# Performance work log

Measured on AMD Instinct MI355X. Metric: run time of the kernel, lower is better.

The kernel has to match this reference:

```python
import jax, jax.numpy as jnp
import numpy as np

LAMBDA1 = 0.3366
LAMBDA2 = 0.2424
LAMBDA3 = 0.06
LR = 0.1
N_ITERS = 10          # fixed iteration count standing in for the eps-based while loop
BETA1, BETA2, ADAM_EPS = 0.9, 0.999, 1e-8


def setup_inputs() -> dict:
    key = jax.random.key(0)
    k1, k2, k3 = jax.random.split(key, 3)
    D, T, K = 512, 50000, 16
    return {
        "embedding": jax.random.normal(k1, (D, T), jnp.float32),
        "basis_init": jax.random.normal(k2, (D, K), jnp.float32),
        "activation_init": jax.random.normal(k3, (K, T), jnp.float32),
        "k": K,
    }


def _matrix_l1(X):
    # torch.linalg.norm(X, ord=1) on a 2D tensor = induced 1-norm = max column abs-sum
    return jnp.max(jnp.sum(jnp.abs(X), axis=0))


def _jitter(A):
    # temporal jitter penalty: sum of abs frame-to-frame differences
    return jnp.sum(jnp.abs(A[:, 1:] - A[:, :-1]))


def _shrink(X):
    # faithful to the (buggy) torch _shrink: sign(X) * max(0, |X - lr*l|)
    return jnp.sign(X) * jnp.maximum(0.0, jnp.abs(X - LR * LAMBDA1))


def _adam(p, g, m, v, t):
    m = BETA1 * m + (1.0 - BETA1) * g
    v = BETA2 * v + (1.0 - BETA2) * g * g
    mh = m / (1.0 - BETA1 ** t)
    vh = v / (1.0 - BETA2 ** t)
    p = p - LR * mh / (jnp.sqrt(vh) + ADAM_EPS)
    return p, m, v


def _run(embedding, basis_init, activation_init):
    A = activation_init  # optimizer_act.step() is never called in the source -> A is constant

    def loss_from_B(B):
        return (_matrix_l1(embedding - B @ A)
                + LAMBDA1 * _matrix_l1(B)
                + LAMBDA2 * _matrix_l1(A)
                + LAMBDA3 * _jitter(A))

    # iteration 1: loss is computed on the raw parameter (shrink applied after the step)
    P = basis_init
    m = jnp.zeros_like(P)
    v = jnp.zeros_like(P)
    g = jax.grad(loss_from_B)(P)
    P, m, v = _adam(P, g, m, v, jnp.float32(1.0))

    # iterations 2..N: loss sees shrink(P); gradient flows through the shrink into P
    def step(carry, t):
        P, m, v = carry
        g = jax.grad(lambda p: loss_from_B(_shrink(p)))(P)
        P, m, v = _adam(P, g, m, v, t)
        return (P, m, v), None

    ts = jnp.arange(2, N_ITERS + 1, dtype=jnp.float32)
    (P, m, v), _ = jax.lax.scan(step, (P, m, v), ts)
    return _shrink(P), A


def reference(embedding, basis_init, activation_init, k):
    # returns (embedding_basis_matrix, activation_matrix) as in OutputDiarization
    return _run(embedding, basis_init, activation_init)
```

## Files before the change

### kernel.cpp

```cpp
#include <hip/hip_runtime.h>
#include <hip/hip_cooperative_groups.h>

namespace cg = cooperative_groups;

#define D 512
#define T 50000
#define K 16
#define NIT 10

#define NBLK 256
#define BTH  512
#define COLS_PER_BLOCK 196
#define NGRP 49
#define PASSES 2

#define LAMBDA1 0.3366f
#define LR      0.1f
#define SHRINK_C (LR * LAMBDA1)
#define BETA1   0.9f
#define BETA2   0.999f
#define ADAM_EPS 1e-8f

__device__ __forceinline__ float sgn(float x) {
    return (x > 0.f) ? 1.f : ((x < 0.f) ? -1.f : 0.f);
}

__global__ __launch_bounds__(BTH, 2) void diar_all(
        const float* __restrict__ E, const float* __restrict__ Bin,
        const float* __restrict__ A, float* __restrict__ out,
        unsigned long long* __restrict__ slot) {
    __shared__ __align__(16) float Bl[D * K];
    __shared__ float4 psum[16][32];
    __shared__ float wsum[8][K];
    __shared__ float colA[K];
    __shared__ int js_s, ks_s;

    const int tid = threadIdx.x;
    const int bid = blockIdx.x;
    cg::grid_group grid = cg::this_grid();

    float pr[K], mr[K], vr[K];
    {
        const float4* src = reinterpret_cast<const float4*>(Bin + tid * K);
        float4* bl4 = reinterpret_cast<float4*>(&Bl[tid * K]);
#pragma unroll
        for (int q = 0; q < 4; ++q) {
            float4 x = src[q];
            bl4[q] = x;
            pr[4 * q + 0] = x.x; pr[4 * q + 1] = x.y;
            pr[4 * q + 2] = x.z; pr[4 * q + 3] = x.w;
        }
#pragma unroll
        for (int k = 0; k < K; ++k) { mr[k] = 0.f; vr[k] = 0.f; }
    }
    if (bid == 0 && tid < NIT) atomicExch(&slot[tid], 0ull);
    __syncthreads();
    grid.sync();

    const int c = tid & 31;
    const int s = tid >> 5;

    float b1p = 1.f, b2p = 1.f;

    for (int it = 1; it <= NIT; ++it) {
        b1p *= BETA1; b2p *= BETA2;

        unsigned long long key = 0ull;
#pragma unroll
        for (int p = 0; p < PASSES; ++p) {
            const int g = p * 32 + c;
            const int j0 = bid * COLS_PER_BLOCK + g * 4;
            const bool ok = (g < NGRP) && (j0 < T);
            float4 acc = {0.f, 0.f, 0.f, 0.f};
            if (ok) {
                float4 a4[K];
#pragma unroll
                for (int k = 0; k < K; ++k)
                    a4[k] = *reinterpret_cast<const float4*>(A + (size_t)k * T + j0);
                const int rbase = s * 32;
                const float* Ep = E + j0;
#pragma unroll 4
                for (int ii = 0; ii < 32; ++ii) {
                    const int i = rbase + ii;
                    const float4 e = *reinterpret_cast<const float4*>(Ep + (size_t)i * T);
                    const float4* br = reinterpret_cast<const float4*>(&Bl[i * K]);
                    float bb[K];
                    *reinterpret_cast<float4*>(&bb[0])  = br[0];
                    *reinterpret_cast<float4*>(&bb[4])  = br[1];
                    *reinterpret_cast<float4*>(&bb[8])  = br[2];
                    *reinterpret_cast<float4*>(&bb[12]) = br[3];
                    float4 r = e;
#pragma unroll
                    for (int k = 0; k < K; ++k) {
                        r.x = fmaf(-bb[k], a4[k].x, r.x);
                        r.y = fmaf(-bb[k], a4[k].y, r.y);
                        r.z = fmaf(-bb[k], a4[k].z, r.z);
                        r.w = fmaf(-bb[k], a4[k].w, r.w);
                    }
                    acc.x += fabsf(r.x); acc.y += fabsf(r.y);
                    acc.z += fabsf(r.z); acc.w += fabsf(r.w);
                }
            }
            psum[s][c] = acc;
            __syncthreads();
            if (tid < 32) {
                const int gg = p * 32 + tid;
                const int jb = bid * COLS_PER_BLOCK + gg * 4;
                if (gg < NGRP && jb < T) {
                    float4 cs = psum[0][tid];
#pragma unroll
                    for (int q = 1; q < 16; ++q) {
                        float4 pq = psum[q][tid];
                        cs.x += pq.x; cs.y += pq.y; cs.z += pq.z; cs.w += pq.w;
                    }
                    float v4[4] = {cs.x, cs.y, cs.z, cs.w};
#pragma unroll
                    for (int q = 0; q < 4; ++q) {
                        unsigned long long kq =
                            (((unsigned long long)__float_as_uint(v4[q])) << 32)
                            | (unsigned int)(jb + q);
                        if (kq > key) key = kq;
                    }
                }
            }
            __syncthreads();
        }
        if (tid < 64) {
#pragma unroll
            for (int off = 32; off > 0; off >>= 1) {
                unsigned long long o = __shfl_down(key, off, 64);
                if (o > key) key = o;
            }
            if (tid == 0) atomicMax(&slot[it - 1], key);
        }

        grid.sync();

        if (tid == 0) {
            unsigned long long kk = atomicMax(&slot[it - 1], 0ull);
            js_s = (int)(kk & 0xffffffffull);
        }
        __syncthreads();
        const int js = js_s;
        if (tid < K) colA[tid] = A[(size_t)tid * T + js];

        float cb[K];
        {
            const float* brow = &Bl[tid * K];
#pragma unroll
            for (int k = 0; k < K; ++k) cb[k] = fabsf(brow[k]);
#pragma unroll
            for (int off = 32; off > 0; off >>= 1) {
#pragma unroll
                for (int k = 0; k < K; ++k) cb[k] += __shfl_down(cb[k], off, 64);
            }
            if ((tid & 63) == 0) {
                const int w = tid >> 6;
#pragma unroll
                for (int k = 0; k < K; ++k) wsum[w][k] = cb[k];
            }
        }
        __syncthreads();
        if (tid == 0) {
            float best = -1.f; int kb = 0;
#pragma unroll
            for (int k = 0; k < K; ++k) {
                float t = 0.f;
                for (int w = 0; w < 8; ++w) t += wsum[w][k];
                if (t > best) { best = t; kb = k; }
            }
            ks_s = kb;
        }
        __syncthreads();
        const int ks = ks_s;
        const float biasm = 1.f - b1p;
        const float biasv = 1.f - b2p;

        float r = E[(size_t)tid * T + js];
        const float* brow = &Bl[tid * K];
#pragma unroll
        for (int k = 0; k < K; ++k) r = fmaf(-brow[k], colA[k], r);
        const float sg = sgn(r);

#pragma unroll
        for (int k = 0; k < K; ++k) {
            float g = -sg * colA[k];
            if (k == ks) g += LAMBDA1 * sgn(brow[k]);
            float p = pr[k];
            if (it >= 2) g *= sgn(p) * sgn(p - SHRINK_C);
            float mm = BETA1 * mr[k] + (1.f - BETA1) * g;
            float vv = BETA2 * vr[k] + (1.f - BETA2) * g * g;
            mr[k] = mm; vr[k] = vv;
            p -= LR * (mm / biasm) / (sqrtf(vv / biasv) + ADAM_EPS);
            pr[k] = p;
        }
        {
            float4* bl4 = reinterpret_cast<float4*>(&Bl[tid * K]);
#pragma unroll
            for (int q = 0; q < 4; ++q) {
                float4 x;
                x.x = sgn(pr[4 * q + 0]) * fmaxf(0.f, fabsf(pr[4 * q + 0] - SHRINK_C));
                x.y = sgn(pr[4 * q + 1]) * fmaxf(0.f, fabsf(pr[4 * q + 1] - SHRINK_C));
                x.z = sgn(pr[4 * q + 2]) * fmaxf(0.f, fabsf(pr[4 * q + 2] - SHRINK_C));
                x.w = sgn(pr[4 * q + 3]) * fmaxf(0.f, fabsf(pr[4 * q + 3] - SHRINK_C));
                bl4[q] = x;
            }
        }
        __syncthreads();
    }

    if (bid == 0) {
        float4* o4 = reinterpret_cast<float4*>(out);
        const float4* b4 = reinterpret_cast<const float4*>(Bl);
#pragma unroll
        for (int q = 0; q < 4; ++q) o4[tid * 4 + q] = b4[tid * 4 + q];
    }
    {
        float4* o4 = reinterpret_cast<float4*>(out) + (D * K) / 4;
        const float4* a4p = reinterpret_cast<const float4*>(A);
        const int n4 = (K * T) / 4;
        for (int q = bid * BTH + tid; q < n4; q += NBLK * BTH) o4[q] = a4p[q];
    }
}

extern "C" void kernel_launch(void* const* d_in, const int* in_sizes, int n_in,
                              void* d_out, int out_size, void* d_ws, size_t ws_size,
                              hipStream_t stream) {
    const float* E   = (const float*)d_in[0];
    const float* Bin = (const float*)d_in[1];
    const float* A   = (const float*)d_in[2];
    float* out = (float*)d_out;
    unsigned long long* slot = (unsigned long long*)d_ws;

    void* args[] = { (void*)&E, (void*)&Bin, (void*)&A, (void*)&out, (void*)&slot };
    hipLaunchCooperativeKernel((void*)diar_all, dim3(NBLK), dim3(BTH),
                               args, 0, stream);
}
```

Baseline: 860.0 us.

## Stage each block's embedding tile contiguously in workspace for later iterations

On the first iteration each block writes its strided slice of the embedding into a private, densely packed tile in workspace (row stride 196 floats instead of T). Iterations 2..N read from this compact tile, which is meant to improve locality and let the ~400KB per-block tile hit in L2/MALL rather than streaming the full strided matrix each time. This adds a full write of the embedding in the first iteration and needs about 100MB of workspace, with no check on ws_size.

```diff
diff --git a/kernel.cpp b/kernel.cpp
--- a/kernel.cpp
+++ b/kernel.cpp
@@ -13,6 +13,8 @@
 #define COLS_PER_BLOCK 196
 #define NGRP 49
 #define PASSES 2
+#define TILE_LD 196
+#define TILE_FLOATS (D * TILE_LD)
 
 #define LAMBDA1 0.3366f
 #define LR      0.1f
@@ -25,10 +27,29 @@
     return (x > 0.f) ? 1.f : ((x < 0.f) ? -1.f : 0.f);
 }
 
+__device__ __forceinline__ void accum_row(const float4 e, const float* __restrict__ brow,
+                                          const float4* __restrict__ a4, float4& acc) {
+    float bb[K];
+    *reinterpret_cast<float4*>(&bb[0])  = reinterpret_cast<const float4*>(brow)[0];
+    *reinterpret_cast<float4*>(&bb[4])  = reinterpret_cast<const float4*>(brow)[1];
+    *reinterpret_cast<float4*>(&bb[8])  = reinterpret_cast<const float4*>(brow)[2];
+    *reinterpret_cast<float4*>(&bb[12]) = reinterpret_cast<const float4*>(brow)[3];
+    float4 r = e;
+#pragma unroll
+    for (int k = 0; k < K; ++k) {
+        r.x = fmaf(-bb[k], a4[k].x, r.x);
+        r.y = fmaf(-bb[k], a4[k].y, r.y);
+        r.z = fmaf(-bb[k], a4[k].z, r.z);
+        r.w = fmaf(-bb[k], a4[k].w, r.w);
+    }
+    acc.x += fabsf(r.x); acc.y += fabsf(r.y);
+    acc.z += fabsf(r.z); acc.w += fabsf(r.w);
+}
+
 __global__ __launch_bounds__(BTH, 2) void diar_all(
         const float* __restrict__ E, const float* __restrict__ Bin,
         const float* __restrict__ A, float* __restrict__ out,
-        unsigned long long* __restrict__ slot) {
+        unsigned long long* __restrict__ slot, float* __restrict__ Et) {
     __shared__ __align__(16) float Bl[D * K];
     __shared__ float4 psum[16][32];
     __shared__ float wsum[8][K];
@@ -59,6 +80,7 @@
 
     const int c = tid & 31;
     const int s = tid >> 5;
+    float* const tileB = Et + (size_t)bid * TILE_FLOATS;
 
     float b1p = 1.f, b2p = 1.f;
 
@@ -78,27 +100,24 @@
                 for (int k = 0; k < K; ++k)
                     a4[k] = *reinterpret_cast<const float4*>(A + (size_t)k * T + j0);
                 const int rbase = s * 32;
-                const float* Ep = E + j0;
+                if (it == 1) {
+                    const float* Ep = E + j0;
+                    float* tw = tileB + g * 4;
 #pragma unroll 4
-                for (int ii = 0; ii < 32; ++ii) {
-                    const int i = rbase + ii;
-                    const float4 e = *reinterpret_cast<const float4*>(Ep + (size_t)i * T);
-                    const float4* br = reinterpret_cast<const float4*>(&Bl[i * K]);
-                    float bb[K];
-                    *reinterpret_cast<float4*>(&bb[0])  = br[0];
-                    *reinterpret_cast<float4*>(&bb[4])  = br[1];
-                    *reinterpret_cast<float4*>(&bb[8])  = br[2];
-                    *reinterpret_cast<float4*>(&bb[12]) = br[3];
-                    float4 r = e;
-#pragma unroll
-                    for (int k = 0; k < K; ++k) {
-                        r.x = fmaf(-bb[k], a4[k].x, r.x);
-                        r.y = fmaf(-bb[k], a4[k].y, r.y);
-                        r.z = fmaf(-bb[k], a4[k].z, r.z);
-                        r.w = fmaf(-bb[k], a4[k].w, r.w);
-                    }
-                    acc.x += fabsf(r.x); acc.y += fabsf(r.y);
-                    acc.z += fabsf(r.z); acc.w += fabsf(r.w);
+                    for (int ii = 0; ii < 32; ++ii) {
+                        const int i = rbase + ii;
+                        const float4 e = *reinterpret_cast<const float4*>(Ep + (size_t)i * T);
+                        *reinterpret_cast<float4*>(tw + i * TILE_LD) = e;
+                        accum_row(e, &Bl[i * K], a4, acc);
+                    }
+                } else {
+                    const float* tr = tileB + g * 4;
+#pragma unroll 4
+                    for (int ii = 0; ii < 32; ++ii) {
+                        const int i = rbase + ii;
+                        const float4 e = *reinterpret_cast<const float4*>(tr + i * TILE_LD);
+                        accum_row(e, &Bl[i * K], a4, acc);
+                    }
                 }
             }
             psum[s][c] = acc;
@@ -231,8 +250,10 @@
     const float* A   = (const float*)d_in[2];
     float* out = (float*)d_out;
     unsigned long long* slot = (unsigned long long*)d_ws;
-
-    void* args[] = { (void*)&E, (void*)&Bin, (void*)&A, (void*)&out, (void*)&slot };
+    float* Et = (float*)((char*)d_ws + 1024);
+
+    void* args[] = { (void*)&E, (void*)&Bin, (void*)&A, (void*)&out,
+                     (void*)&slot, (void*)&Et };
     hipLaunchCooperativeKernel((void*)diar_all, dim3(NBLK), dim3(BTH),
                                args, 0, stream);
 }
```

Result: slower. 906.7 us (+5.4%).
